# Performance work log

Measured on AMD Instinct MI355X. Metric: run time of the kernel, lower is better.

## Reference

```python
import jax, jax.numpy as jnp
import numpy as np
from jax import lax

B, NROI, DF, G, EMB, NH, HD, FFD, DEPTH = 8, 400, 512, 25, 360, 4, 90, 2048, 2
KS, ST = 3, 2
EPS = 1e-5


def setup_inputs() -> dict:
    key = jax.random.key(0)
    ks = jax.random.split(key, 16)
    n = lambda i, shp, s=0.02: jax.random.normal(ks[i], shp, jnp.float32) * s
    return {
        "F_roi": jax.random.normal(ks[0], (B, NROI, DF), jnp.float32),
        "C": jax.random.randint(ks[1], (B, G, G, G), 0, NROI + 1),
        "ffn_w1": n(2, (DF, 450)), "ffn_b1": jnp.zeros((450,), jnp.float32),
        "ffn_w2": n(3, (450, EMB)), "ffn_b2": jnp.zeros((EMB,), jnp.float32),
        "wqkv": n(4, (DEPTH, EMB, 3 * EMB)), "bqkv": jnp.zeros((DEPTH, 3 * EMB), jnp.float32),
        "wo": n(5, (DEPTH, EMB, EMB)), "bo": jnp.zeros((DEPTH, EMB), jnp.float32),
        "ln1_s": jnp.ones((DEPTH, EMB), jnp.float32), "ln1_b": jnp.zeros((DEPTH, EMB), jnp.float32),
        "wf1": n(6, (DEPTH, EMB, FFD)), "bf1": jnp.zeros((DEPTH, FFD), jnp.float32),
        "wf2": n(7, (DEPTH, FFD, EMB)), "bf2": jnp.zeros((DEPTH, EMB), jnp.float32),
        "ln2_s": jnp.ones((DEPTH, EMB), jnp.float32), "ln2_b": jnp.zeros((DEPTH, EMB), jnp.float32),
        "cw1": n(8, (EMB, 256)), "cb1": jnp.zeros((256,), jnp.float32),
        "cw2": n(9, (256, 128)), "cb2": jnp.zeros((128,), jnp.float32),
        "cw3": n(10, (128, 2)), "cb3": jnp.zeros((2,), jnp.float32),
    }


def _gelu(x):
    return jax.nn.gelu(x, approximate=False)  # torch default exact GELU


def _ln(x, s, b):
    m = x.mean(-1, keepdims=True)
    v = ((x - m) ** 2).mean(-1, keepdims=True)
    return (x - m) * lax.rsqrt(v + EPS) * s + b


def _mha(x, wqkv, bqkv, wo, bo):
    Bt, T, D = x.shape
    qkv = x @ wqkv + bqkv  # (B,T,3D)
    q, k, v = [t.reshape(Bt, T, NH, HD).transpose(0, 2, 1, 3) for t in jnp.split(qkv, 3, -1)]
    scale = jnp.asarray(1.0 / np.sqrt(HD), x.dtype)
    a = jax.nn.softmax(jnp.einsum('bhqd,bhkd->bhqk', q, k) * scale, axis=-1)
    o = jnp.einsum('bhqk,bhkd->bhqd', a, v).transpose(0, 2, 1, 3).reshape(Bt, T, D)
    return o @ wo + bo


def _nodes(F_roi, C, ffn_w1, ffn_b1, ffn_w2, ffn_b2):
    # FFN embed (dropout off in eval)
    F_emb = _gelu(F_roi @ ffn_w1 + ffn_b1) @ ffn_w2 + ffn_b2  # (B,NROI,EMB)
    # construct_brain_map: gather dense voxel grid, index 0 -> zero padding row
    F_pad = jnp.concatenate([jnp.zeros((B, 1, EMB), F_emb.dtype), F_emb], axis=1)
    Q = F_pad[jnp.arange(B)[:, None, None, None], C]  # (B,G,G,G,EMB)
    # extract_nodes: unfold 3x3x3 / stride-2 box-sum == reduce_window sum
    blk = lax.reduce_window(Q, 0.0, lax.add, (1, KS, KS, KS, 1), (1, ST, ST, ST, 1), 'VALID')
    return blk.reshape(B, -1, EMB)  # (B, n_blocks, EMB)


def _encode(tokens, wqkv, bqkv, wo, bo, ln1_s, ln1_b, wf1, bf1, wf2, bf2, ln2_s, ln2_b,
            cw1, cb1, cw2, cb2, cw3, cb3):
    x = tokens
    for l in range(DEPTH):  # post-norm TransformerEncoderLayer, GELU, dropout off
        x = _ln(x + _mha(x, wqkv[l], bqkv[l], wo[l], bo[l]), ln1_s[l], ln1_b[l])
        x = _ln(x + (_gelu(x @ wf1[l] + bf1[l]) @ wf2[l] + bf2[l]), ln2_s[l], ln2_b[l])
    h = x.mean(axis=1)  # DEC (external, unavailable) treated as identity pass-through
    h = _gelu(h @ cw1 + cb1)
    h = jax.nn.relu(h @ cw2 + cb2)
    return h @ cw3 + cb3  # (B, num_classes)


def reference(F_roi, C, ffn_w1, ffn_b1, ffn_w2, ffn_b2, wqkv, bqkv, wo, bo,
              ln1_s, ln1_b, wf1, bf1, wf2, bf2, ln2_s, ln2_b,
              cw1, cb1, cw2, cb2, cw3, cb3):
    nodes = _nodes(F_roi, C, ffn_w1, ffn_b1, ffn_w2, ffn_b2)
    mask = jnp.abs(nodes).sum(axis=(0, 2)) > 0  # dynamic compaction of nonzero nodes
    valid = jnp.nonzero(mask)[0]
    tokens = nodes[:, valid, :]
    return _encode(tokens, wqkv, bqkv, wo, bo, ln1_s, ln1_b, wf1, bf1, wf2, bf2,
                   ln2_s, ln2_b, cw1, cb1, cw2, cb2, cw3, cb3)
```

## Files before the change

kernel.cpp:

```cpp
#include <hip/hip_runtime.h>
#include <math.h>

#define NB   8
#define NROI 400
#define GG   25
#define EMBD 360
#define HDD  90
#define TBM  1728
#define MTOK 13824

typedef __attribute__((ext_vector_type(8)))  _Float16 h8;
typedef __attribute__((ext_vector_type(4)))  _Float16 h4;
typedef __attribute__((ext_vector_type(16))) float f32x16;

#define MFMA16(a,b,c) __builtin_amdgcn_mfma_f32_32x32x16_f16(a,b,c,0,0,0)
#define QSCALE 0.105409255338945984f

__device__ __forceinline__ float gelu_f(float x) {
    return 0.5f * x * (1.0f + erff(x * 0.7071067811865475f));
}

__global__ __launch_bounds__(256) void k_wconv(
    const float* __restrict__ W, int K, int N,
    _Float16* __restrict__ Wt, int Kp, int Np, int Wls, int Wtls)
{
    W  += (size_t)blockIdx.z * Wls;
    Wt += (size_t)blockIdx.z * Wtls;
    __shared__ float tile[32][33];
    const int k0 = blockIdx.x * 32, n0 = blockIdx.y * 32;
    const int t = threadIdx.x;
    #pragma unroll
    for (int it = 0; it < 4; ++it) {
        int e = t + it * 256;
        int i = e >> 5, j = e & 31;
        tile[j][i] = (k0 + i < K && n0 + j < N) ? W[(size_t)(k0 + i) * N + n0 + j] : 0.0f;
    }
    __syncthreads();
    #pragma unroll
    for (int it = 0; it < 4; ++it) {
        int e = t + it * 256;
        int n = e >> 5, kk = e & 31;
        if (n0 + n < Np && k0 + kk < Kp)
            Wt[(size_t)(n0 + n) * Kp + k0 + kk] = (_Float16)tile[n][kk];
    }
}

__global__ __launch_bounds__(256) void k_wmisc(
    const float* __restrict__ wqkv, const float* __restrict__ wo,
    const float* __restrict__ bqkv,
    _Float16* __restrict__ qkvc, _Float16* __restrict__ woc,
    float* __restrict__ bqp)
{
    int id = blockIdx.x * 256 + threadIdx.x;
    if (id < 884736) {
        int l = id / 442368, r = id - l * 442368;
        int np = r / 384, kk = r - np * 384;
        int sec = np / 384, rr = np - sec * 384, h = rr / 96, d = rr - h * 96;
        float v = 0.0f;
        if (d < HDD && kk < 360) v = wqkv[(size_t)l * 388800 + (size_t)kk * 1080 + sec * 360 + h * HDD + d];
        if (sec == 0) v *= QSCALE;
        qkvc[id] = (_Float16)v;
    } else if (id < 1179648) {
        int r2 = id - 884736;
        int l = r2 / 147456, r = r2 - l * 147456;
        int n = r / 384, kp = r - n * 384;
        int h = kp / 96, d = kp - h * 96;
        float v = 0.0f;
        if (d < HDD && n < 360) v = wo[(size_t)l * 129600 + (size_t)(h * HDD + d) * 360 + n];
        woc[r2] = (_Float16)v;
    } else if (id < 1181952) {
        int r3 = id - 1179648;
        int l = r3 / 1152, r = r3 - l * 1152;
        int sec = r / 384, rr = r - sec * 384, h = rr / 96, d = rr - h * 96;
        float v = 0.0f;
        if (d < HDD) v = bqkv[l * 1080 + sec * 360 + h * HDD + d];
        if (sec == 0) v *= QSCALE;
        if (sec == 2 && d == HDD) v = 1.0f;
        bqp[r3] = v;
    }
}

__global__ __launch_bounds__(256) void k_vtr(
    const _Float16* __restrict__ qkvh, _Float16* __restrict__ vT)
{
    __shared__ _Float16 tile[32][33];
    const int t = threadIdx.x;
    const int tok0 = blockIdx.x * 32;
    const int d0 = blockIdx.y * 32;
    const int bh = blockIdx.z;
    const int b = bh >> 2, h = bh & 3;
    const size_t src = ((size_t)b * TBM + tok0) * 1152 + 768 + 96 * h + d0;
    #pragma unroll
    for (int it = 0; it < 4; ++it) {
        int tl = (t >> 5) + it * 8, dl = t & 31;
        tile[tl][dl] = qkvh[src + (size_t)tl * 1152 + dl];
    }
    __syncthreads();
    const size_t dst = ((size_t)bh * 96 + d0) * TBM + tok0;
    #pragma unroll
    for (int it = 0; it < 4; ++it) {
        int dl = (t >> 5) + it * 8, tl = t & 31;
        vT[dst + (size_t)dl * TBM + tl] = tile[tl][dl];
    }
}

template <int ACT, bool RES, bool OUTH, bool AH>
__global__ __launch_bounds__(256, 3) void k_mgemm(
    const void* __restrict__ Ap, const _Float16* __restrict__ Bt,
    const float* __restrict__ bias, const float* res, void* Cp,
    int M, int N, int K, int Kp)
{
    __shared__ __align__(16) _Float16 Ah[4096], Bh[4096];
    const int t = threadIdx.x;
    const int lane = t & 63, wid = t >> 6;
    const int half = lane >> 5, l31 = lane & 31;
    const int m0 = blockIdx.y * 128, n0 = blockIdx.x * 128;
    const int wm = (wid >> 1) * 64, wn = (wid & 1) * 64;

    f32x16 acc00 = {}, acc01 = {}, acc10 = {}, acc11 = {};
    const int nk = Kp >> 5;
    const bool k4 = (K & 3) == 0;

    h8 acur[2], anxt[2], bcur[2], bnxt[2];
    float4 fcur[4], fnxt[4];

    const _Float16* Af = (const _Float16*)Ap;
    const float* A = (const float*)Ap;

    auto loadA_h = [&](int k0, h8* dst) {
        #pragma unroll
        for (int i = 0; i < 2; ++i) {
            int e = t + i * 256;
            int row = e >> 2, c = e & 3;
            int gm = m0 + row; if (gm > M - 1) gm = M - 1;
            dst[i] = *(const h8*)(Af + (size_t)gm * Kp + k0 + c * 8);
        }
    };
    auto loadA_f = [&](int k0, float4* dst) {
        #pragma unroll
        for (int i = 0; i < 4; ++i) {
            int e = t + i * 256;
            int row = e >> 3, c4 = e & 7;
            int gm = m0 + row, kb = k0 + c4 * 4;
            float4 fv = {0.f, 0.f, 0.f, 0.f};
            if (gm < M) {
                const float* ap = A + (size_t)gm * K + kb;
                if (k4 && kb + 3 < K) {
                    fv = *(const float4*)ap;
                } else {
                    if (kb + 0 < K) fv.x = ap[0];
                    if (kb + 1 < K) fv.y = ap[1];
                    if (kb + 2 < K) fv.z = ap[2];
                    if (kb + 3 < K) fv.w = ap[3];
                }
            }
            dst[i] = fv;
        }
    };
    auto loadB = [&](int k0, h8* dst) {
        #pragma unroll
        for (int i = 0; i < 2; ++i) {
            int e = t + i * 256;
            int col = e >> 2, c = e & 3;
            dst[i] = *(const h8*)(Bt + (size_t)(n0 + col) * Kp + k0 + c * 8);
        }
    };

    if (AH) loadA_h(0, acur); else loadA_f(0, fcur);
    loadB(0, bcur);

    for (int ks = 0; ks < nk; ++ks) {
        const bool pf = (ks + 1 < nk);
        if (pf) {
            if (AH) loadA_h((ks + 1) << 5, anxt); else loadA_f((ks + 1) << 5, fnxt);
            loadB((ks + 1) << 5, bnxt);
        }
        __syncthreads();
        if (AH) {
            #pragma unroll
            for (int i = 0; i < 2; ++i) {
                int e = t + i * 256;
                int row = e >> 2, c = e & 3;
                *(h8*)&Ah[(c * 128 + row) * 8] = acur[i];
            }
        } else {
            #pragma unroll
            for (int i = 0; i < 4; ++i) {
                int e = t + i * 256;
                int row = e >> 3, c4 = e & 7;
                float4 fv = fcur[i];
                h4 hv = { (_Float16)fv.x, (_Float16)fv.y, (_Float16)fv.z, (_Float16)fv.w };
                int c = c4 >> 1, sub = c4 & 1;
                *(h4*)&Ah[(c * 128 + row) * 8 + sub * 4] = hv;
            }
        }
        #pragma unroll
        for (int i = 0; i < 2; ++i) {
            int e = t + i * 256;
            int col = e >> 2, c = e & 3;
            *(h8*)&Bh[(c * 128 + col) * 8] = bcur[i];
        }
        __syncthreads();
        h8 af[2][2], bf[2][2];
        #pragma unroll
        for (int m2 = 0; m2 < 2; ++m2)
            #pragma unroll
            for (int ku = 0; ku < 2; ++ku) {
                int c = ku * 2 + half;
                af[m2][ku] = *(const h8*)&Ah[(c * 128 + wm + m2 * 32 + l31) * 8];
                bf[m2][ku] = *(const h8*)&Bh[(c * 128 + wn + m2 * 32 + l31) * 8];
            }
        #pragma unroll
        for (int ku = 0; ku < 2; ++ku) {
            acc00 = MFMA16(af[0][ku], bf[0][ku], acc00);
            acc01 = MFMA16(af[0][ku], bf[1][ku], acc01);
            acc10 = MFMA16(af[1][ku], bf[0][ku], acc10);
            acc11 = MFMA16(af[1][ku], bf[1][ku], acc11);
        }
        if (pf) {
            if (AH) { acur[0] = anxt[0]; acur[1] = anxt[1]; }
            else    { fcur[0] = fnxt[0]; fcur[1] = fnxt[1]; fcur[2] = fnxt[2]; fcur[3] = fnxt[3]; }
            bcur[0] = bnxt[0]; bcur[1] = bnxt[1];
        }
    }
    float* Cf = (float*)Cp;
    _Float16* Ch = (_Float16*)Cp;
    #define EPILOG(ACCV, M2, N2) { \
        int gn = n0 + wn + (N2) * 32 + l31; \
        if (gn < N) { \
            float bv = bias[gn]; \
            _Pragma("unroll") \
            for (int r = 0; r < 16; ++r) { \
                int gm = m0 + wm + (M2) * 32 + (r & 3) + 8 * (r >> 2) + 4 * half; \
                if (gm < M) { \
                    float v = ACCV[r] + bv; \
                    if (RES) v += res[(size_t)gm * N + gn]; \
                    if (ACT == 1) v = gelu_f(v); \
                    if (OUTH) Ch[(size_t)gm * N + gn] = (_Float16)v; \
                    else      Cf[(size_t)gm * N + gn] = v; \
                } } } }
    EPILOG(acc00, 0, 0) EPILOG(acc01, 0, 1) EPILOG(acc10, 1, 0) EPILOG(acc11, 1, 1)
    #undef EPILOG
}

__global__ __launch_bounds__(256, 3) void k_skgemm(
    const _Float16* __restrict__ A, const _Float16* __restrict__ Bt,
    float* __restrict__ P, int Kp, int KCH, int nstep)
{
    __shared__ __align__(16) _Float16 Ah[4096], Bh[4096];
    const int t = threadIdx.x;
    const int lane = t & 63, wid = t >> 6;
    const int half = lane >> 5, l31 = lane & 31;
    const int m0 = blockIdx.y * 128, n0 = blockIdx.x * 128;
    const int wm = (wid >> 1) * 64, wn = (wid & 1) * 64;
    const int zb = blockIdx.z * KCH;
    P += (size_t)blockIdx.z * MTOK * EMBD;

    f32x16 acc00 = {}, acc01 = {}, acc10 = {}, acc11 = {};

    h8 acur[2], anxt[2], bcur[2], bnxt[2];
    auto loadA = [&](int k0, h8* dst) {
        #pragma unroll
        for (int i = 0; i < 2; ++i) {
            int e = t + i * 256;
            int row = e >> 2, c = e & 3;
            dst[i] = *(const h8*)(A + (size_t)(m0 + row) * Kp + k0 + c * 8);
        }
    };
    auto loadB = [&](int k0, h8* dst) {
        #pragma unroll
        for (int i = 0; i < 2; ++i) {
            int e = t + i * 256;
            int col = e >> 2, c = e & 3;
            dst[i] = *(const h8*)(Bt + (size_t)(n0 + col) * Kp + k0 + c * 8);
        }
    };

    loadA(zb, acur); loadB(zb, bcur);

    for (int ks = 0; ks < nstep; ++ks) {
        const bool pf = (ks + 1 < nstep);
        if (pf) { loadA(zb + ((ks + 1) << 5), anxt); loadB(zb + ((ks + 1) << 5), bnxt); }
        __syncthreads();
        #pragma unroll
        for (int i = 0; i < 2; ++i) {
            int e = t + i * 256;
            int row = e >> 2, c = e & 3;
            *(h8*)&Ah[(c * 128 + row) * 8] = acur[i];
        }
        #pragma unroll
        for (int i = 0; i < 2; ++i) {
            int e = t + i * 256;
            int col = e >> 2, c = e & 3;
            *(h8*)&Bh[(c * 128 + col) * 8] = bcur[i];
        }
        __syncthreads();
        h8 af[2][2], bf[2][2];
        #pragma unroll
        for (int m2 = 0; m2 < 2; ++m2)
            #pragma unroll
            for (int ku = 0; ku < 2; ++ku) {
                int c = ku * 2 + half;
                af[m2][ku] = *(const h8*)&Ah[(c * 128 + wm + m2 * 32 + l31) * 8];
                bf[m2][ku] = *(const h8*)&Bh[(c * 128 + wn + m2 * 32 + l31) * 8];
            }
        #pragma unroll
        for (int ku = 0; ku < 2; ++ku) {
            acc00 = MFMA16(af[0][ku], bf[0][ku], acc00);
            acc01 = MFMA16(af[0][ku], bf[1][ku], acc01);
            acc10 = MFMA16(af[1][ku], bf[0][ku], acc10);
            acc11 = MFMA16(af[1][ku], bf[1][ku], acc11);
        }
        if (pf) { acur[0] = anxt[0]; acur[1] = anxt[1]; bcur[0] = bnxt[0]; bcur[1] = bnxt[1]; }
    }
    #define EPILOGP(ACCV, M2, N2) { \
        int gn = n0 + wn + (N2) * 32 + l31; \
        if (gn < EMBD) { \
            _Pragma("unroll") \
            for (int r = 0; r < 16; ++r) { \
                int gm = m0 + wm + (M2) * 32 + (r & 3) + 8 * (r >> 2) + 4 * half; \
                P[(size_t)gm * EMBD + gn] = ACCV[r]; \
            } } }
    EPILOGP(acc00, 0, 0) EPILOGP(acc01, 0, 1) EPILOGP(acc10, 1, 0) EPILOGP(acc11, 1, 1)
    #undef EPILOGP
}

__global__ __launch_bounds__(256, 2) void k_mattn(
    const _Float16* __restrict__ qkv, const _Float16* __restrict__ vT,
    _Float16* __restrict__ aob, const int* __restrict__ tcp)
{
    __shared__ __align__(16) _Float16 Kl[64 * 128];
    __shared__ __align__(16) _Float16 Vl[6144];
    __shared__ __align__(16) _Float16 Pl[4][32 * 64];

    const int t = threadIdx.x;
    const int lane = t & 63, wid = t >> 6;
    const int half = lane >> 5, l31 = lane & 31;
    const int bid = blockIdx.x;
    const int bh = bid & 31, qt = bid >> 5;
    const int h = bh & 3, b = bh >> 2;
    const int Tc = *tcp;
    const int q0w = qt * 128 + wid * 32;
    const size_t base = (size_t)b * TBM * 1152 + 96 * h;
    const _Float16* vTb = vT + (size_t)bh * 96 * TBM;

    int skk[3], scc[3], sdd[3], smm[3];
    #pragma unroll
    for (int i = 0; i < 3; ++i) {
        int cid = t + i * 256;
        skk[i] = cid / 12; scc[i] = cid - skk[i] * 12;
        sdd[i] = cid >> 3; smm[i] = cid & 7;
    }

    h8 qf[6];
    {
        int rl = q0w + l31; if (rl > TBM - 1) rl = TBM - 1;
        const _Float16* qrow = qkv + base + (size_t)rl * 1152;
        #pragma unroll
        for (int ku = 0; ku < 6; ++ku)
            qf[ku] = *(const h8*)(qrow + ku * 16 + half * 8);
    }

    f32x16 o0 = {}, o1 = {}, o2 = {};
    int nkt = (Tc + 63) >> 6; if (nkt > 27) nkt = 27;

    if (nkt > 0) {
        #pragma unroll
        for (int i = 0; i < 3; ++i) {
            *(h8*)&Kl[skk[i] * 128 + ((scc[i] ^ (skk[i] & 7)) << 3)] =
                *(const h8*)(qkv + base + (size_t)skk[i] * 1152 + 384 + scc[i] * 8);
            *(h8*)&Vl[sdd[i] * 64 + ((smm[i] ^ (sdd[i] & 7)) << 3)] =
                *(const h8*)(vTb + (size_t)sdd[i] * TBM + smm[i] * 8);
        }
    }
    __syncthreads();

    for (int kt = 0; kt < nkt; ++kt) {
        const int k0 = kt * 64;
        h8 kpre[3], vpre[3];
        const bool pf = (kt + 1 < nkt);
        if (pf) {
            #pragma unroll
            for (int i = 0; i < 3; ++i) {
                kpre[i] = *(const h8*)(qkv + base + (size_t)(k0 + 64 + skk[i]) * 1152 + 384 + scc[i] * 8);
                vpre[i] = *(const h8*)(vTb + (size_t)sdd[i] * TBM + k0 + 64 + smm[i] * 8);
            }
        }
        f32x16 s0 = {}, s1 = {};
        #pragma unroll
        for (int ku = 0; ku < 6; ++ku) {
            int c = ku * 2 + half;
            int cp = c ^ (l31 & 7);
            h8 kb0 = *(const h8*)&Kl[l31 * 128 + cp * 8];
            h8 kb1 = *(const h8*)&Kl[(32 + l31) * 128 + cp * 8];
            s0 = MFMA16(qf[ku], kb0, s0);
            s1 = MFMA16(qf[ku], kb1, s1);
        }
        const bool ok0 = (k0 + l31) < Tc;
        const bool ok1 = (k0 + 32 + l31) < Tc;
        const int c0 = l31 >> 3, c1 = 4 + (l31 >> 3), j0 = l31 & 7;
        #pragma unroll
        for (int r = 0; r < 16; ++r) {
            int ql = (r & 3) + 8 * (r >> 2) + 4 * half;
            float p0v = ok0 ? __expf(s0[r]) : 0.0f;
            float p1v = ok1 ? __expf(s1[r]) : 0.0f;
            Pl[wid][ql * 64 + (c0 ^ (ql & 7)) * 8 + j0] = (_Float16)p0v;
            Pl[wid][ql * 64 + (c1 ^ (ql & 7)) * 8 + j0] = (_Float16)p1v;
        }
        asm volatile("s_waitcnt lgkmcnt(0)" ::: "memory");
        __builtin_amdgcn_sched_barrier(0);
        h8 pa[4];
        #pragma unroll
        for (int ku = 0; ku < 4; ++ku) {
            int c = ku * 2 + half;
            pa[ku] = *(const h8*)&Pl[wid][l31 * 64 + (c ^ (l31 & 7)) * 8];
        }
        #pragma unroll
        for (int n = 0; n < 3; ++n) {
            f32x16* op = n == 0 ? &o0 : (n == 1 ? &o1 : &o2);
            int d = n * 32 + l31;
            #pragma unroll
            for (int ku = 0; ku < 4; ++ku) {
                int m = ku * 2 + half;
                h8 vb = *(const h8*)&Vl[d * 64 + ((m ^ (d & 7)) << 3)];
                *op = MFMA16(pa[ku], vb, *op);
            }
        }
        __syncthreads();
        if (pf) {
            #pragma unroll
            for (int i = 0; i < 3; ++i) {
                *(h8*)&Kl[skk[i] * 128 + ((scc[i] ^ (skk[i] & 7)) << 3)] = kpre[i];
                *(h8*)&Vl[sdd[i] * 64 + ((smm[i] ^ (sdd[i] & 7)) << 3)] = vpre[i];
            }
        }
        __syncthreads();
    }

    #pragma unroll
    for (int r = 0; r < 16; ++r) {
        float den = __shfl(o2[r], (lane & 32) | 26);
        float inv = (den > 0.0f) ? 1.0f / den : 0.0f;
        int qg = q0w + (r & 3) + 8 * (r >> 2) + 4 * half;
        if (qg < Tc) {
            _Float16* orow = aob + ((size_t)b * TBM + qg) * 384 + 96 * h;
            orow[l31]      = (_Float16)(o0[r] * inv);
            orow[32 + l31] = (_Float16)(o1[r] * inv);
            orow[64 + l31] = (64 + l31 < HDD) ? (_Float16)(o2[r] * inv) : (_Float16)0.0f;
        }
    }
}

__global__ __launch_bounds__(128) void k_pool(
    const float* __restrict__ F_emb, const int* __restrict__ C,
    float* __restrict__ nodes, float* __restrict__ vsum)
{
    const int tkn = blockIdx.x, b = blockIdx.y;
    const int oz = tkn % 12, oy = (tkn / 12) % 12, ox = tkn / 144;
    __shared__ int idx[27];
    const int tid = threadIdx.x;
    if (tid < 27) {
        int dx = tid / 9, dy = (tid / 3) % 3, dz = tid % 3;
        idx[tid] = C[(((b * GG) + ox * 2 + dx) * GG + oy * 2 + dy) * GG + oz * 2 + dz];
    }
    __syncthreads();
    float a0 = 0.f, a1 = 0.f, a2 = 0.f;
    for (int n = 0; n < 27; ++n) {
        int c = idx[n];
        if (c == 0) continue;
        const float* src = F_emb + (size_t)(b * NROI + (c - 1)) * EMBD;
        a0 += src[tid]; a1 += src[tid + 128];
        if (tid < 104) a2 += src[tid + 256];
    }
    float* dst = nodes + ((size_t)b * TBM + tkn) * EMBD;
    dst[tid] = a0; dst[tid + 128] = a1;
    if (tid < 104) dst[tid + 256] = a2;
    float s = fabsf(a0) + fabsf(a1) + ((tid < 104) ? fabsf(a2) : 0.0f);
    #pragma unroll
    for (int o = 32; o >= 1; o >>= 1) s += __shfl_xor(s, o);
    __shared__ float red[2];
    if ((tid & 63) == 0) red[tid >> 6] = s;
    __syncthreads();
    if (tid == 0) atomicAdd(&vsum[tkn], red[0] + red[1]);
}

__global__ __launch_bounds__(256) void k_scan(
    const float* __restrict__ vsum, int* __restrict__ cidx, int* __restrict__ tcp)
{
    __shared__ int csum[256];
    __shared__ int coff[256];
    const int t = threadIdx.x;
    const int base = t * 7;
    int loc[7]; int s = 0;
    #pragma unroll
    for (int i = 0; i < 7; ++i) {
        int g = base + i;
        int v = (g < TBM) ? (vsum[g] > 0.0f ? 1 : 0) : 0;
        loc[i] = v; s += v;
    }
    csum[t] = s;
    __syncthreads();
    if (t == 0) {
        int a = 0;
        for (int i = 0; i < 256; ++i) { coff[i] = a; a += csum[i]; }
        *tcp = a;
    }
    __syncthreads();
    int off = coff[t];
    #pragma unroll
    for (int i = 0; i < 7; ++i) {
        int g = base + i;
        if (g < TBM && loc[i]) cidx[off++] = g;
    }
}

__global__ __launch_bounds__(128) void k_compact(
    const float* __restrict__ nodes, const int* __restrict__ cidx,
    const int* __restrict__ tcp, float* __restrict__ xf, _Float16* __restrict__ xh)
{
    const int j = blockIdx.x, b = blockIdx.y;
    const int Tc = *tcp;
    const size_t row = (size_t)b * TBM + j;
    const float* src = (j < Tc) ? nodes + ((size_t)b * TBM + cidx[j]) * EMBD : nullptr;
    for (int e = threadIdx.x; e < 384; e += 128) {
        float v = (e < EMBD && src) ? src[e] : 0.0f;
        if (e < EMBD) xf[row * EMBD + e] = v;
        xh[row * 384 + e] = (_Float16)v;
    }
}

__global__ __launch_bounds__(256) void k_lnr(
    const float* __restrict__ p0, const float* __restrict__ p1,
    const float* __restrict__ bias, const float* res,
    const float* __restrict__ sc, const float* __restrict__ bc,
    float* outf, _Float16* __restrict__ outh)
{
    const int lane = threadIdx.x & 63;
    const int row = blockIdx.x * 4 + (threadIdx.x >> 6);
    const size_t ro = (size_t)row * EMBD;
    const int e0 = lane * 6;
    float x[6] = {0.f, 0.f, 0.f, 0.f, 0.f, 0.f};
    float sum = 0.f;
    if (lane < 60) {
        #pragma unroll
        for (int i = 0; i < 6; ++i) {
            float v = p0[ro + e0 + i] + p1[ro + e0 + i] + bias[e0 + i] + res[ro + e0 + i];
            x[i] = v; sum += v;
        }
    }
    #pragma unroll
    for (int o = 32; o >= 1; o >>= 1) sum += __shfl_xor(sum, o);
    const float mean = sum * (1.0f / 360.0f);
    float vs = 0.f;
    if (lane < 60) {
        #pragma unroll
        for (int i = 0; i < 6; ++i) { float d = x[i] - mean; vs += d * d; }
    }
    #pragma unroll
    for (int o = 32; o >= 1; o >>= 1) vs += __shfl_xor(vs, o);
    const float rs = rsqrtf(vs * (1.0f / 360.0f) + 1e-5f);
    _Float16* hrow = outh + (size_t)row * 384;
    if (lane < 60) {
        #pragma unroll
        for (int i = 0; i < 6; ++i) {
            float v = (x[i] - mean) * rs * sc[e0 + i] + bc[e0 + i];
            outf[ro + e0 + i] = v;
            hrow[e0 + i] = (_Float16)v;
        }
    } else {
        #pragma unroll
        for (int i = 0; i < 6; ++i)
            hrow[360 + (lane - 60) * 6 + i] = (_Float16)0.0f;
    }
}

__global__ __launch_bounds__(128) void k_mean2(
    const float* __restrict__ x, float* __restrict__ partial,
    const int* __restrict__ tcp)
{
    const int chunk = blockIdx.x;
    const int b = blockIdx.y;
    const int t = threadIdx.x;
    const int Tc = *tcp;
    int j0 = chunk * 108;
    int j1 = j0 + 108; if (j1 > Tc) j1 = Tc;
    const float* xb = x + (size_t)b * TBM * EMBD;
    float a0 = 0.f, a1 = 0.f, a2 = 0.f;
    for (int j = j0; j < j1; ++j) {
        const float* r = xb + (size_t)j * EMBD;
        a0 += r[t]; a1 += r[t + 128];
        if (t < 104) a2 += r[t + 256];
    }
    float* p = partial + ((size_t)chunk * NB + b) * EMBD;
    p[t] = a0; p[t + 128] = a1;
    if (t < 104) p[t + 256] = a2;
}

__global__ __launch_bounds__(256) void k_head(
    const float* __restrict__ partial, const int* __restrict__ tcp,
    const float* __restrict__ cw1, const float* __restrict__ cb1,
    const float* __restrict__ cw2, const float* __restrict__ cb2,
    const float* __restrict__ cw3, const float* __restrict__ cb3,
    float* __restrict__ outp)
{
    const int b = blockIdx.x;
    __shared__ float hs[EMBD];
    __shared__ float h1[256];
    __shared__ float h2[128];
    const int t = threadIdx.x;
    int Tc = *tcp; if (Tc < 1) Tc = 1;
    const float inv = 1.0f / (float)Tc;
    for (int e = t; e < EMBD; e += 256) {
        float s = 0.f;
        #pragma unroll
        for (int c = 0; c < 16; ++c) s += partial[(size_t)c * NB * EMBD + b * EMBD + e];
        hs[e] = s * inv;
    }
    __syncthreads();
    {
        float s = cb1[t];
        for (int k = 0; k < EMBD; ++k) s = fmaf(hs[k], cw1[k * 256 + t], s);
        h1[t] = gelu_f(s);
    }
    __syncthreads();
    if (t < 128) {
        float s = cb2[t];
        for (int k = 0; k < 256; ++k) s = fmaf(h1[k], cw2[k * 128 + t], s);
        h2[t] = fmaxf(s, 0.0f);
    }
    __syncthreads();
    if (t < 2) {
        float s = cb3[t];
        for (int k = 0; k < 128; ++k) s = fmaf(h2[k], cw3[k * 2 + t], s);
        outp[b * 2 + t] = s;
    }
}

extern "C" void kernel_launch(void* const* d_in, const int* in_sizes, int n_in,
                              void* d_out, int out_size, void* d_ws, size_t ws_size,
                              hipStream_t stream)
{
    const float* F_roi  = (const float*)d_in[0];
    const int*   C      = (const int*)d_in[1];
    const float* ffn_w1 = (const float*)d_in[2];
    const float* ffn_b1 = (const float*)d_in[3];
    const float* ffn_w2 = (const float*)d_in[4];
    const float* ffn_b2 = (const float*)d_in[5];
    const float* wqkv   = (const float*)d_in[6];
    const float* bqkv   = (const float*)d_in[7];
    const float* wo     = (const float*)d_in[8];
    const float* bo     = (const float*)d_in[9];
    const float* ln1s   = (const float*)d_in[10];
    const float* ln1b   = (const float*)d_in[11];
    const float* wf1    = (const float*)d_in[12];
    const float* bf1    = (const float*)d_in[13];
    const float* wf2    = (const float*)d_in[14];
    const float* bf2    = (const float*)d_in[15];
    const float* ln2s   = (const float*)d_in[16];
    const float* ln2b   = (const float*)d_in[17];
    const float* cw1    = (const float*)d_in[18];
    const float* cb1    = (const float*)d_in[19];
    const float* cw2    = (const float*)d_in[20];
    const float* cb2    = (const float*)d_in[21];
    const float* cw3    = (const float*)d_in[22];
    const float* cb3    = (const float*)d_in[23];
    float* out = (float*)d_out;

    float* ws = (float*)d_ws;
    _Float16* qkvh = (_Float16*)ws;
    float*    tmp450 = ws;
    float*    F_emb  = ws + 1440000;
    float*    midf   = ws + 7962624;
    _Float16* midb   = (_Float16*)midf;
    float*    nodes  = midf;
    _Float16* aob    = (_Float16*)(ws + 22118400);
    float*    p0     = ws + 24772608;
    float*    p1     = ws + 29749248;
    float*    t360   = ws + 34725888;
    _Float16* xh     = (_Float16*)(ws + 39702528);
    _Float16* sw     = (_Float16*)(ws + 42356736);

    size_t so = 0;
    auto salloc = [&](size_t n) { _Float16* p = sw + so; so += n; return p; };
    _Float16* w1c  = salloc(262144);
    _Float16* w2c  = salloc(184320);
    _Float16* qkvc = salloc(2 * 442368);
    _Float16* woc  = salloc(2 * 147456);
    _Float16* f1c  = salloc(2 * 786432);
    _Float16* f2c  = salloc(2 * 786432);
    float* partial = ws + 44742656;
    int*   ints    = (int*)(partial + 46080);
    int*   cidx    = ints;
    int*   tcp     = ints + 1728;
    float* vsumf   = (float*)(ints + 1732);
    float* bqp     = vsumf + 1728;
    _Float16* vT   = (_Float16*)(ws + 44800000);

    dim3 blk(256);

    k_wconv<<<dim3(16, 16, 1), blk, 0, stream>>>(ffn_w1, 512, 450, w1c, 512, 512, 0, 0);
    k_wconv<<<dim3(15, 12, 1), blk, 0, stream>>>(ffn_w2, 450, 360, w2c, 480, 384, 0, 0);
    k_wconv<<<dim3(12, 64, 2), blk, 0, stream>>>(wf1, 360, 2048, f1c, 384, 2048, 360 * 2048, 786432);
    k_wconv<<<dim3(64, 12, 2), blk, 0, stream>>>(wf2, 2048, 360, f2c, 2048, 384, 2048 * 360, 786432);
    k_wmisc<<<dim3(4618), blk, 0, stream>>>(wqkv, wo, bqkv, qkvc, woc, bqp);

    hipMemsetAsync(vsumf, 0, TBM * sizeof(float), stream);
    k_mgemm<1, false, false, false><<<dim3(4, 25), blk, 0, stream>>>(F_roi, w1c, ffn_b1, nullptr, tmp450, 3200, 450, 512, 512);
    k_mgemm<0, false, false, false><<<dim3(3, 25), blk, 0, stream>>>(tmp450, w2c, ffn_b2, nullptr, F_emb, 3200, 360, 450, 480);
    k_pool<<<dim3(1728, 8), dim3(128), 0, stream>>>(F_emb, C, nodes, vsumf);
    k_scan<<<dim3(1), blk, 0, stream>>>(vsumf, cidx, tcp);
    k_compact<<<dim3(1728, 8), dim3(128), 0, stream>>>(nodes, cidx, tcp, t360, xh);

    for (int l = 0; l < 2; ++l) {
        k_mgemm<0, false, true, true><<<dim3(9, 108), blk, 0, stream>>>(xh, qkvc + (size_t)l * 442368, bqp + l * 1152, nullptr, qkvh, MTOK, 1152, 360, 384);
        k_vtr<<<dim3(54, 3, 32), blk, 0, stream>>>(qkvh, vT);
        k_mattn<<<dim3(448), blk, 0, stream>>>(qkvh, vT, aob, tcp);
        k_skgemm<<<dim3(3, 108, 2), blk, 0, stream>>>(aob, woc + (size_t)l * 147456, p0, 384, 192, 6);
        k_lnr<<<dim3(MTOK / 4), blk, 0, stream>>>(p0, p1, bo + l * 360, t360, ln1s + l * 360, ln1b + l * 360, t360, xh);
        k_mgemm<1, false, true, true><<<dim3(16, 108), blk, 0, stream>>>(xh, f1c + (size_t)l * 786432, bf1 + l * 2048, nullptr, midb, MTOK, 2048, 360, 384);
        k_skgemm<<<dim3(3, 108, 2), blk, 0, stream>>>(midb, f2c + (size_t)l * 786432, p0, 2048, 1024, 32);
        k_lnr<<<dim3(MTOK / 4), blk, 0, stream>>>(p0, p1, bf2 + l * 360, t360, ln2s + l * 360, ln2b + l * 360, t360, xh);
    }

    k_mean2<<<dim3(16, 8), dim3(128), 0, stream>>>(t360, partial, tcp);
    k_head<<<dim3(8), blk, 0, stream>>>(partial, tcp, cw1, cb1, cw2, cb2, cw3, cb3, out);
}
```

Before: 680.8 us.

## Keep attention probabilities in registers and double-buffer K/V tiles

The attention kernel now computes S transposed (K as the A operand) so each lane holds a row of scores. It converts those scores to fp16 pairs and exchanges halves with v_permlane32_swap, forming the P operand for the PV MFMA directly. This removes the per-wave shared-memory P buffer and its write/read round trip. K and V tiles are now double-buffered in LDS, which removes one of the two __syncthreads per key tile, at the cost of more LDS per block (possibly lower occupancy).

After: 666.6 us. 2.1% less time.

```diff
diff --git a/kernel.cpp b/kernel.cpp
--- a/kernel.cpp
+++ b/kernel.cpp
@@ -12,6 +12,7 @@
 typedef __attribute__((ext_vector_type(8)))  _Float16 h8;
 typedef __attribute__((ext_vector_type(4)))  _Float16 h4;
 typedef __attribute__((ext_vector_type(16))) float f32x16;
+typedef __attribute__((ext_vector_type(4)))  unsigned u32x4;
 
 #define MFMA16(a,b,c) __builtin_amdgcn_mfma_f32_32x32x16_f16(a,b,c,0,0,0)
 #define QSCALE 0.105409255338945984f
@@ -329,9 +330,8 @@
     const _Float16* __restrict__ qkv, const _Float16* __restrict__ vT,
     _Float16* __restrict__ aob, const int* __restrict__ tcp)
 {
-    __shared__ __align__(16) _Float16 Kl[64 * 128];
-    __shared__ __align__(16) _Float16 Vl[6144];
-    __shared__ __align__(16) _Float16 Pl[4][32 * 64];
+    __shared__ __align__(16) _Float16 Kl[2][8192];
+    __shared__ __align__(16) _Float16 Vl[2][6144];
 
     const int t = threadIdx.x;
     const int lane = t & 63, wid = t >> 6;
@@ -345,11 +345,14 @@
     const _Float16* vTb = vT + (size_t)bh * 96 * TBM;
 
     int skk[3], scc[3], sdd[3], smm[3];
+    int koff[3], voff[3];
     #pragma unroll
     for (int i = 0; i < 3; ++i) {
         int cid = t + i * 256;
         skk[i] = cid / 12; scc[i] = cid - skk[i] * 12;
         sdd[i] = cid >> 3; smm[i] = cid & 7;
+        koff[i] = skk[i] * 128 + ((scc[i] ^ (skk[i] & 7)) << 3);
+        voff[i] = sdd[i] * 64 + ((smm[i] ^ (sdd[i] & 7)) << 3);
     }
 
     h8 qf[6];
@@ -367,9 +370,9 @@
     if (nkt > 0) {
         #pragma unroll
         for (int i = 0; i < 3; ++i) {
-            *(h8*)&Kl[skk[i] * 128 + ((scc[i] ^ (skk[i] & 7)) << 3)] =
+            *(h8*)&Kl[0][koff[i]] =
                 *(const h8*)(qkv + base + (size_t)skk[i] * 1152 + 384 + scc[i] * 8);
-            *(h8*)&Vl[sdd[i] * 64 + ((smm[i] ^ (sdd[i] & 7)) << 3)] =
+            *(h8*)&Vl[0][voff[i]] =
                 *(const h8*)(vTb + (size_t)sdd[i] * TBM + smm[i] * 8);
         }
     }
@@ -377,6 +380,7 @@
 
     for (int kt = 0; kt < nkt; ++kt) {
         const int k0 = kt * 64;
+        const int cur = kt & 1, nxt = cur ^ 1;
         h8 kpre[3], vpre[3];
         const bool pf = (kt + 1 < nkt);
         if (pf) {
@@ -386,34 +390,39 @@
                 vpre[i] = *(const h8*)(vTb + (size_t)sdd[i] * TBM + k0 + 64 + smm[i] * 8);
             }
         }
-        f32x16 s0 = {}, s1 = {};
+        f32x16 sT0 = {}, sT1 = {};
         #pragma unroll
         for (int ku = 0; ku < 6; ++ku) {
             int c = ku * 2 + half;
             int cp = c ^ (l31 & 7);
-            h8 kb0 = *(const h8*)&Kl[l31 * 128 + cp * 8];
-            h8 kb1 = *(const h8*)&Kl[(32 + l31) * 128 + cp * 8];
-            s0 = MFMA16(qf[ku], kb0, s0);
-            s1 = MFMA16(qf[ku], kb1, s1);
-        }
-        const bool ok0 = (k0 + l31) < Tc;
-        const bool ok1 = (k0 + 32 + l31) < Tc;
-        const int c0 = l31 >> 3, c1 = 4 + (l31 >> 3), j0 = l31 & 7;
-        #pragma unroll
-        for (int r = 0; r < 16; ++r) {
-            int ql = (r & 3) + 8 * (r >> 2) + 4 * half;
-            float p0v = ok0 ? __expf(s0[r]) : 0.0f;
-            float p1v = ok1 ? __expf(s1[r]) : 0.0f;
-            Pl[wid][ql * 64 + (c0 ^ (ql & 7)) * 8 + j0] = (_Float16)p0v;
-            Pl[wid][ql * 64 + (c1 ^ (ql & 7)) * 8 + j0] = (_Float16)p1v;
-        }
-        asm volatile("s_waitcnt lgkmcnt(0)" ::: "memory");
-        __builtin_amdgcn_sched_barrier(0);
+            h8 kb0 = *(const h8*)&Kl[cur][l31 * 128 + cp * 8];
+            h8 kb1 = *(const h8*)&Kl[cur][(32 + l31) * 128 + cp * 8];
+            sT0 = MFMA16(kb0, qf[ku], sT0);
+            sT1 = MFMA16(kb1, qf[ku], sT1);
+        }
         h8 pa[4];
         #pragma unroll
-        for (int ku = 0; ku < 4; ++ku) {
-            int c = ku * 2 + half;
-            pa[ku] = *(const h8*)&Pl[wid][l31 * 64 + (c ^ (l31 & 7)) * 8];
+        for (int g = 0; g < 2; ++g) {
+            const f32x16& sT = g ? sT1 : sT0;
+            const int kbase = k0 + g * 32;
+            unsigned w0, w1, w2, w3, w4, w5, w6, w7;
+            #define CVTW(W, R0, R1) { \
+                int ka = kbase + ((R0) & 3) + 8 * ((R0) >> 2) + 4 * half; \
+                int kb_ = kbase + ((R1) & 3) + 8 * ((R1) >> 2) + 4 * half; \
+                float pva = (ka  < Tc) ? __expf(sT[R0]) : 0.0f; \
+                float pvb = (kb_ < Tc) ? __expf(sT[R1]) : 0.0f; \
+                W = __builtin_bit_cast(unsigned, __builtin_amdgcn_cvt_pkrtz(pva, pvb)); }
+            CVTW(w0, 0, 1)  CVTW(w1, 2, 3)  CVTW(w2, 4, 5)  CVTW(w3, 6, 7)
+            CVTW(w4, 8, 9)  CVTW(w5, 10, 11) CVTW(w6, 12, 13) CVTW(w7, 14, 15)
+            #undef CVTW
+            asm volatile("v_permlane32_swap_b32 %0, %1" : "+v"(w0), "+v"(w2));
+            asm volatile("v_permlane32_swap_b32 %0, %1" : "+v"(w1), "+v"(w3));
+            asm volatile("v_permlane32_swap_b32 %0, %1" : "+v"(w4), "+v"(w6));
+            asm volatile("v_permlane32_swap_b32 %0, %1" : "+v"(w5), "+v"(w7));
+            u32x4 lo = { w0, w1, w2, w3 };
+            u32x4 hi = { w4, w5, w6, w7 };
+            pa[g * 2 + 0] = __builtin_bit_cast(h8, lo);
+            pa[g * 2 + 1] = __builtin_bit_cast(h8, hi);
         }
         #pragma unroll
         for (int n = 0; n < 3; ++n) {
@@ -422,16 +431,15 @@
             #pragma unroll
             for (int ku = 0; ku < 4; ++ku) {
                 int m = ku * 2 + half;
-                h8 vb = *(const h8*)&Vl[d * 64 + ((m ^ (d & 7)) << 3)];
+                h8 vb = *(const h8*)&Vl[cur][d * 64 + ((m ^ (d & 7)) << 3)];
                 *op = MFMA16(pa[ku], vb, *op);
             }
         }
-        __syncthreads();
         if (pf) {
             #pragma unroll
             for (int i = 0; i < 3; ++i) {
-                *(h8*)&Kl[skk[i] * 128 + ((scc[i] ^ (skk[i] & 7)) << 3)] = kpre[i];
-                *(h8*)&Vl[sdd[i] * 64 + ((smm[i] ^ (sdd[i] & 7)) << 3)] = vpre[i];
+                *(h8*)&Kl[nxt][koff[i]] = kpre[i];
+                *(h8*)&Vl[nxt][voff[i]] = vpre[i];
             }
         }
         __syncthreads();
@@ -704,7 +712,7 @@
     k_wconv<<<dim3(64, 12, 2), blk, 0, stream>>>(wf2, 2048, 360, f2c, 2048, 384, 2048 * 360, 786432);
     k_wmisc<<<dim3(4618), blk, 0, stream>>>(wqkv, wo, bqkv, qkvc, woc, bqp);
 
-    hipMemsetAsync(vsumf, 0, TBM * sizeof(float), stream);
+    hipError_t e0 = hipMemsetAsync(vsumf, 0, TBM * sizeof(float), stream); (void)e0;
     k_mgemm<1, false, false, false><<<dim3(4, 25), blk, 0, stream>>>(F_roi, w1c, ffn_b1, nullptr, tmp450, 3200, 450, 512, 512);
     k_mgemm<0, false, false, false><<<dim3(3, 25), blk, 0, stream>>>(tmp450, w2c, ffn_b2, nullptr, F_emb, 3200, 360, 450, 480);
     k_pool<<<dim3(1728, 8), dim3(128), 0, stream>>>(F_emb, C, nodes, vsumf);
```
